# Kernel optimization log

Hardware: AMD Instinct MI355X
Metric: run time of the kernel (lower is better)

## Reference

```python
import jax, jax.numpy as jnp
import numpy as np

N_NODES, N_EDGES, NUM_GRAPHS = 50000, 800000, 64
F_DIM, H_DIM, N_LAYERS, N_CLASSES = 64, 64, 3, 16
EPS = 1e-5  # StdAggregation epsilon (PyG)


def setup_inputs() -> dict:
    key = jax.random.key(0)
    ks = jax.random.split(key, 12)
    s = 0.05
    x = jax.random.normal(ks[0], (N_NODES, F_DIM), jnp.float32)
    edge_index = jax.random.randint(ks[1], (2, N_EDGES), 0, N_NODES, dtype=jnp.int32)
    batch = jnp.sort(jax.random.randint(ks[2], (N_NODES,), 0, NUM_GRAPHS, dtype=jnp.int32))
    # per-layer PNAConv params (towers=1): pre Linear(2F->F), post Linear(13F->H), lin Linear(H->H)
    pre_w = jax.random.normal(ks[3], (N_LAYERS, F_DIM, 2 * F_DIM), jnp.float32) * s
    pre_b = jnp.zeros((N_LAYERS, F_DIM), jnp.float32)
    post_w = jax.random.normal(ks[4], (N_LAYERS, H_DIM, 13 * F_DIM), jnp.float32) * s
    post_b = jnp.zeros((N_LAYERS, H_DIM), jnp.float32)
    lin_w = jax.random.normal(ks[5], (N_LAYERS, H_DIM, H_DIM), jnp.float32) * s
    lin_b = jnp.zeros((N_LAYERS, H_DIM), jnp.float32)
    mlp_w1 = jax.random.normal(ks[6], (H_DIM, H_DIM), jnp.float32) * s
    mlp_b1 = jnp.zeros((H_DIM,), jnp.float32)
    mlp_w2 = jax.random.normal(ks[7], (N_CLASSES, H_DIM), jnp.float32) * s
    mlp_b2 = jnp.zeros((N_CLASSES,), jnp.float32)
    return dict(x=x, edge_index=edge_index, batch=batch,
                pre_w=pre_w, pre_b=pre_b, post_w=post_w, post_b=post_b,
                lin_w=lin_w, lin_b=lin_b, mlp_w1=mlp_w1, mlp_b1=mlp_b1,
                mlp_w2=mlp_w2, mlp_b2=mlp_b2)


def pna_forward(x, src, dst, pre_w, pre_b, post_w, post_b, lin_w, lin_b,
                mlp_w1, mlp_b1, mlp_w2, mlp_b2, batch):
    N = x.shape[0]
    deg_raw = jax.ops.segment_sum(jnp.ones_like(src, jnp.float32), dst, N)  # in-degree [N]
    deg = jnp.maximum(deg_raw, 1.0)[:, None]
    # avg log degree (PNA avg_deg['log'] from the degree histogram of this graph)
    avg_log = jnp.mean(jnp.log(deg_raw + 1.0))
    log_deg = jnp.log(deg + 1.0)
    amp = log_deg / avg_log          # amplification scaler [N,1]
    att = avg_log / log_deg          # attenuation scaler [N,1]
    has_in = (deg_raw > 0)[:, None]

    for l in range(pre_w.shape[0]):
        h = jnp.concatenate([x[dst], x[src]], axis=-1)        # [E, 2F] (x_i, x_j)
        m = h @ pre_w[l].T + pre_b[l]                          # pre_nn message [E, F]
        s1 = jax.ops.segment_sum(m, dst, N)
        s2 = jax.ops.segment_sum(m * m, dst, N)
        mean = s1 / deg
        std = jnp.sqrt(jax.nn.relu(s2 / deg - mean * mean) + EPS)
        mn = jnp.where(has_in, jax.ops.segment_min(m, dst, N), 0.0)
        mx = jnp.where(has_in, jax.ops.segment_max(m, dst, N), 0.0)
        aggr = jnp.concatenate([mean, mn, mx, std], axis=-1)   # [N, 4F]
        out = jnp.concatenate([x, aggr, aggr * amp, aggr * att], axis=-1)  # [N, 13F]
        out = out @ post_w[l].T + post_b[l]                    # post_nn [N, H]
        x = jax.nn.relu(out @ lin_w[l].T + lin_b[l])           # conv.lin + outer ReLU

    # global mean pool over graphs
    counts = jnp.maximum(
        jax.ops.segment_sum(jnp.ones((N,), x.dtype), batch, NUM_GRAPHS), 1.0)
    g = jax.ops.segment_sum(x, batch, NUM_GRAPHS) / counts[:, None]  # [G, H]
    g = jax.nn.relu(g @ mlp_w1.T + mlp_b1)
    return g @ mlp_w2.T + mlp_b2                               # [G, C]


def reference(x, edge_index, batch, pre_w, pre_b, post_w, post_b,
              lin_w, lin_b, mlp_w1, mlp_b1, mlp_w2, mlp_b2):
    src, dst = edge_index[0], edge_index[1]
    return pna_forward(x, src, dst, pre_w, pre_b, post_w, post_b,
                       lin_w, lin_b, mlp_w1, mlp_b1, mlp_w2, mlp_b2, batch)
```

## Files before the change

kernel.cpp:

```cpp
#include <hip/hip_runtime.h>
#include <math.h>

#define N_NODES   50000
#define N_EDGES   800000
#define NUM_GRAPHS 64
#define FDIM      64
#define HDIM      64
#define NLAYERS   3
#define NCLASSES  16
#define EPS       1e-5f

#define SCAN_CHUNK 1024
#define NCHUNKS ((N_NODES + SCAN_CHUNK - 1) / SCAN_CHUNK)

typedef unsigned short u16;
typedef unsigned int   u32;
typedef __attribute__((ext_vector_type(8))) short short8;
typedef __attribute__((ext_vector_type(4))) float floatx4;

#define WKS_LAYER 159744

__device__ inline void split1(float f, u16& h, u16& m, u16& l) {
    u32 b  = __float_as_uint(f);
    u32 hb = b & 0xFFFF0000u;
    float r = f - __uint_as_float(hb);
    u32 mb = __float_as_uint(r) & 0xFFFF0000u;
    float r2 = r - __uint_as_float(mb);
    u32 lb = __float_as_uint(r2) & 0xFFFF0000u;
    h = (u16)(hb >> 16); m = (u16)(mb >> 16); l = (u16)(lb >> 16);
}

__device__ inline void gl_lds16(const void* g, void* l) {
    __builtin_amdgcn_global_load_lds(
        (const __attribute__((address_space(1))) u32*)g,
        (__attribute__((address_space(3))) u32*)l, 16, 0, 0);
}

__global__ __launch_bounds__(256) void k_comb(const float* __restrict__ post_w,
                                              const float* __restrict__ lin_w,
                                              const float* __restrict__ post_b,
                                              const float* __restrict__ lin_b,
                                              u16* __restrict__ WkS,
                                              float* __restrict__ bcv,
                                              int* __restrict__ cnt,
                                              float* __restrict__ logsum) {
    int b = blockIdx.x, t = threadIdx.x;
    int zi = b * 256 + t;
    if (zi < N_NODES) cnt[zi] = 0;
    if (zi == 0) *logsum = 0.f;

    if (b < 624) {
        int c  = t & 63;
        int kl = t >> 6;
        int l  = b / 208;
        int o  = (b % 208) * 4 + kl;
        const float* lw = lin_w + (size_t)l * 4096 + c * 64;
        const float* pw = post_w + (size_t)l * 53248 + o;
        float acc = 0.f;
        #pragma unroll 8
        for (int j = 0; j < 64; ++j)
            acc += lw[j] * pw[(size_t)j * 832];
        u16 h, m, lo;
        split1(acc, h, m, lo);

        int kn;
        if (o < 64) kn = o;
        else {
            int s  = (o - 64) >> 8;
            int mm = (o - 64) & 255;
            int j  = mm >> 5, r = mm & 31;
            kn = 64 + j * 96 + s * 32 + r;
        }
        int ch  = kn >> 5;
        int kin = kn & 31;
        int n16 = c & 15, nt = c >> 4;
        int swk = (((kin >> 3) + (n16 >> 1)) & 3) * 8 + (kin & 7);
        size_t base = (size_t)l * WKS_LAYER + (size_t)ch * 6144
                    + nt * 512 + n16 * 32 + swk;
        WkS[base]        = h;
        WkS[base + 2048] = m;
        WkS[base + 4096] = lo;
    } else if (t < 192) {
        int l = t >> 6, c = t & 63;
        float acc = lin_b[l * 64 + c];
        for (int j = 0; j < 64; ++j)
            acc += lin_w[(size_t)l * 4096 + c * 64 + j] * post_b[l * 64 + j];
        bcv[l * 64 + c] = acc;
    }
}

__global__ void k_count(const int* __restrict__ dst, int* __restrict__ cnt,
                        int* __restrict__ rank) {
    int e = blockIdx.x * 256 + threadIdx.x;
    if (e < N_EDGES) rank[e] = atomicAdd(&cnt[dst[e]], 1);
}

__global__ void k_chunk_sums(const int* __restrict__ cnt, int* __restrict__ bsum,
                             float* __restrict__ logsum) {
    __shared__ int   ired[256];
    __shared__ float lred[256];
    int b = blockIdx.x, t = threadIdx.x;
    int base = b * SCAN_CHUNK;
    int s = 0; float ls = 0.f;
    for (int i = t; i < SCAN_CHUNK; i += 256) {
        int idx = base + i;
        if (idx < N_NODES) {
            int v = cnt[idx];
            s += v;
            ls += logf((float)v + 1.0f);
        }
    }
    ired[t] = s; lred[t] = ls;
    __syncthreads();
    for (int off = 128; off > 0; off >>= 1) {
        if (t < off) { ired[t] += ired[t + off]; lred[t] += lred[t + off]; }
        __syncthreads();
    }
    if (t == 0) { bsum[b] = ired[0]; atomicAdd(logsum, lred[0]); }
}

__global__ void k_scan_top(const int* __restrict__ bsum, int* __restrict__ boff,
                           int* __restrict__ row_start) {
    if (threadIdx.x == 0) {
        int acc = 0;
        for (int i = 0; i < NCHUNKS; ++i) { boff[i] = acc; acc += bsum[i]; }
        row_start[N_NODES] = acc;
    }
}

__global__ void k_scan_chunks(const int* __restrict__ cnt, const int* __restrict__ boff,
                              int* __restrict__ row_start) {
    __shared__ int tsum[256];
    int b = blockIdx.x, t = threadIdx.x;
    int base = b * SCAN_CHUNK + t * 4;
    int v[4]; int s = 0;
    #pragma unroll
    for (int i = 0; i < 4; ++i) {
        int idx = base + i;
        v[i] = (idx < N_NODES) ? cnt[idx] : 0;
        s += v[i];
    }
    tsum[t] = s;
    __syncthreads();
    for (int off = 1; off < 256; off <<= 1) {
        int val = (t >= off) ? tsum[t - off] : 0;
        __syncthreads();
        tsum[t] += val;
        __syncthreads();
    }
    int excl = boff[b] + tsum[t] - s;
    #pragma unroll
    for (int i = 0; i < 4; ++i) {
        int idx = base + i;
        if (idx < N_NODES) row_start[idx] = excl;
        excl += v[i];
    }
}

__global__ void k_scatter(const int* __restrict__ src, const int* __restrict__ dst,
                          const int* __restrict__ rank,
                          const int* __restrict__ row_start,
                          int* __restrict__ csr_src) {
    int e = blockIdx.x * 256 + threadIdx.x;
    if (e < N_EDGES) {
        int d = dst[e];
        csr_src[row_start[d] + rank[e]] = src[e];
    }
}

__global__ void k_scal(const int* __restrict__ cnt, const float* __restrict__ logsum,
                       float* __restrict__ inv_deg, float* __restrict__ ampv,
                       float* __restrict__ attv, float* __restrict__ g_sum,
                       int* __restrict__ g_cnt) {
    int n = blockIdx.x * 256 + threadIdx.x;
    if (blockIdx.x == 0) {
        for (int i = threadIdx.x; i < 4096; i += 256) g_sum[i] = 0.f;
        if (threadIdx.x < 64) g_cnt[threadIdx.x] = 0;
    }
    if (n < N_NODES) {
        float avg = logsum[0] / (float)N_NODES;
        float degf = fmaxf((float)cnt[n], 1.0f);
        inv_deg[n] = 1.0f / degf;
        float ld = logf(degf + 1.0f);
        ampv[n] = ld / avg;
        attv[n] = avg / ld;
    }
}

__global__ __launch_bounds__(256) void k_pre(const float* __restrict__ x,
                                             const float* __restrict__ pre_w,
                                             const float* __restrict__ pre_b,
                                             float* __restrict__ p,
                                             float* __restrict__ q) {
    __shared__ float At[64][68];
    __shared__ float Wt[128][68];
    int t = threadIdx.x;
    int c4 = (t & 15) * 4;
    int r4 = (t >> 4) * 4;
    int rowBase = blockIdx.x * 64;
    int srow = t >> 2, skq = t & 3;

    #pragma unroll
    for (int pass = 0; pass < 4; ++pass) {
        int kk = (pass * 4 + skq) * 4;
        int row = rowBase + srow;
        float4 v = make_float4(0.f, 0.f, 0.f, 0.f);
        if (row < N_NODES) v = *(const float4*)&x[(size_t)row * 64 + kk];
        At[kk + 0][srow] = v.x;
        At[kk + 1][srow] = v.y;
        At[kk + 2][srow] = v.z;
        At[kk + 3][srow] = v.w;
    }
    for (int idx4 = t; idx4 < 2048; idx4 += 256) {
        int c = idx4 & 63, kq = idx4 >> 6;
        float4 v = *(const float4*)&pre_w[(size_t)c * 128 + kq * 4];
        Wt[kq * 4 + 0][c] = v.x;
        Wt[kq * 4 + 1][c] = v.y;
        Wt[kq * 4 + 2][c] = v.z;
        Wt[kq * 4 + 3][c] = v.w;
    }
    __syncthreads();

    float accp[4][4] = {{0}}, accq[4][4] = {{0}};
    #pragma unroll 4
    for (int kk = 0; kk < 64; ++kk) {
        float4 a  = *(const float4*)&At[kk][r4];
        float4 wp = *(const float4*)&Wt[kk][c4];
        float4 wq = *(const float4*)&Wt[64 + kk][c4];
        float av[4]  = {a.x, a.y, a.z, a.w};
        float wpv[4] = {wp.x, wp.y, wp.z, wp.w};
        float wqv[4] = {wq.x, wq.y, wq.z, wq.w};
        #pragma unroll
        for (int i = 0; i < 4; ++i)
            #pragma unroll
            for (int j = 0; j < 4; ++j) {
                accp[i][j] += av[i] * wpv[j];
                accq[i][j] += av[i] * wqv[j];
            }
    }
    float pb[4];
    #pragma unroll
    for (int j = 0; j < 4; ++j) pb[j] = pre_b[c4 + j];
    #pragma unroll
    for (int i = 0; i < 4; ++i) {
        int row = rowBase + r4 + i;
        if (row < N_NODES) {
            float4 vp = make_float4(accp[i][0] + pb[0], accp[i][1] + pb[1],
                                    accp[i][2] + pb[2], accp[i][3] + pb[3]);
            float4 vq = make_float4(accq[i][0], accq[i][1], accq[i][2], accq[i][3]);
            *(float4*)&p[row * 64 + c4] = vp;
            *(float4*)&q[row * 64 + c4] = vq;
        }
    }
}

__global__ __launch_bounds__(256) void k_aggr(const float* __restrict__ p,
                                              const float* __restrict__ q,
                                              const int* __restrict__ row_start,
                                              const int* __restrict__ csr_src,
                                              const float* __restrict__ inv_deg,
                                              float* __restrict__ aggr) {
    int wid  = (blockIdx.x * 256 + threadIdx.x) >> 6;
    int lane = threadIdx.x & 63;
    if (wid >= N_NODES) return;
    int n = wid;
    int beg = row_start[n], end = row_start[n + 1];
    float sum = 0.f, sq = 0.f;
    float mn = INFINITY, mx = -INFINITY;
    int e = beg;
    for (; e + 7 < end; e += 8) {
        float qv[8];
        #pragma unroll
        for (int u = 0; u < 8; ++u) {
            int s = csr_src[e + u];
            qv[u] = q[(size_t)s * 64 + lane];
        }
        #pragma unroll
        for (int u = 0; u < 8; ++u) {
            float m = qv[u];
            sum += m; sq += m * m;
            mn = fminf(mn, m); mx = fmaxf(mx, m);
        }
    }
    for (; e + 3 < end; e += 4) {
        float qv[4];
        #pragma unroll
        for (int u = 0; u < 4; ++u) {
            int s = csr_src[e + u];
            qv[u] = q[(size_t)s * 64 + lane];
        }
        #pragma unroll
        for (int u = 0; u < 4; ++u) {
            float m = qv[u];
            sum += m; sq += m * m;
            mn = fminf(mn, m); mx = fmaxf(mx, m);
        }
    }
    for (; e < end; ++e) {
        int s = csr_src[e];
        float m = q[(size_t)s * 64 + lane];
        sum += m; sq += m * m;
        mn = fminf(mn, m); mx = fmaxf(mx, m);
    }
    float* a = aggr + (size_t)n * 256;
    if (end <= beg) {
        a[lane]       = 0.f;
        a[64 + lane]  = 0.f;
        a[128 + lane] = 0.f;
        a[192 + lane] = sqrtf(EPS);
    } else {
        float pv = p[n * 64 + lane];
        float id = inv_deg[n];
        float meanq = sum * id;
        float var = fmaxf(sq * id - meanq * meanq, 0.f);
        a[lane]       = pv + meanq;
        a[64 + lane]  = pv + mn;
        a[128 + lane] = pv + mx;
        a[192 + lane] = sqrtf(var + EPS);
    }
}

__global__ __launch_bounds__(256, 4) void k_post(const float* __restrict__ x,
                                                 const float* __restrict__ aggr,
                                                 const float* __restrict__ ampv,
                                                 const float* __restrict__ attv,
                                                 const u16* __restrict__ WkS,
                                                 const float* __restrict__ bc,
                                                 float* __restrict__ xout) {
    __shared__ u16 ldsB[2 * 6144];
    int t = threadIdx.x;
    int w = t >> 6;
    int lane = t & 63;
    int m = lane & 15;
    int qh = lane >> 4;
    int rowBase = blockIdx.x * 64;

    int myrow = rowBase + 16 * w + m;
    bool vr = myrow < N_NODES;
    float ampR = vr ? ampv[myrow] : 0.f;
    float attR = vr ? attv[myrow] : 0.f;
    const float* xrow = x + (size_t)(vr ? myrow : 0) * 64;
    const float* arow = aggr + (size_t)(vr ? myrow : 0) * 256;

    int bo = m * 32 + ((qh + (m >> 1)) & 3) * 8;

    floatx4 acc[4] = {};
    float fc[8], fn[8];
    #pragma unroll
    for (int i = 0; i < 8; ++i) { fc[i] = 0.f; fn[i] = 0.f; }

    auto stageIssue = [&](int ch, int buf) {
        const char* g = (const char*)WkS + (size_t)ch * 12288 + w * 3072 + lane * 16;
        char* l = (char*)ldsB + buf * 12288 + w * 3072;
        #pragma unroll
        for (int i = 0; i < 3; ++i)
            gl_lds16(g + i * 1024, l + i * 1024);
    };
    auto loadRaw = [&](const float* sp, float* f) {
        if (!vr) {
            #pragma unroll
            for (int i = 0; i < 8; ++i) f[i] = 0.f;
            return;
        }
        float4 u0 = *(const float4*)sp;
        float4 u1 = *(const float4*)(sp + 4);
        f[0] = u0.x; f[1] = u0.y; f[2] = u0.z; f[3] = u0.w;
        f[4] = u1.x; f[5] = u1.y; f[6] = u1.z; f[7] = u1.w;
    };

    stageIssue(0, 0);
    loadRaw(xrow + qh * 8, fc);
    asm volatile("s_waitcnt vmcnt(0)" ::: "memory");
    __syncthreads();

    for (int ch = 0; ch < 26; ++ch) {
        if (ch + 1 < 26) stageIssue(ch + 1, (ch + 1) & 1);

        if (ch == 0)      loadRaw(xrow + 32 + qh * 8, fn);
        else if (ch == 1) loadRaw(arow + qh * 8, fn);
        else {
            int j = (ch - 2) / 3, s = (ch - 2) % 3;
            if (s == 2 && j < 7) loadRaw(arow + (j + 1) * 32 + qh * 8, fn);
        }

        float sc = 1.f;
        if (ch >= 2) {
            int s = (ch - 2) % 3;
            sc = (s == 0) ? 1.f : ((s == 1) ? ampR : attR);
        }

        union { u32 u[4]; short8 s8; } AH, AM, AL;
        #pragma unroll
        for (int i = 0; i < 4; ++i) {
            float f0 = fc[2 * i] * sc, f1 = fc[2 * i + 1] * sc;
            u32 b0 = __float_as_uint(f0), b1 = __float_as_uint(f1);
            u32 h0 = b0 & 0xFFFF0000u,  h1 = b1 & 0xFFFF0000u;
            float r0 = f0 - __uint_as_float(h0);
            float r1 = f1 - __uint_as_float(h1);
            u32 m0 = __float_as_uint(r0) & 0xFFFF0000u;
            u32 m1 = __float_as_uint(r1) & 0xFFFF0000u;
            float s0 = r0 - __uint_as_float(m0);
            float s1 = r1 - __uint_as_float(m1);
            u32 l0 = __float_as_uint(s0) & 0xFFFF0000u;
            u32 l1 = __float_as_uint(s1) & 0xFFFF0000u;
            AH.u[i] = (h0 >> 16) | h1;
            AM.u[i] = (m0 >> 16) | m1;
            AL.u[i] = (l0 >> 16) | l1;
        }

        const u16* Bb = ldsB + (ch & 1) * 6144;
        #pragma unroll
        for (int nt = 0; nt < 4; ++nt) {
            short8 bH = *(const short8*)(Bb + nt * 512 + bo);
            short8 bM = *(const short8*)(Bb + 2048 + nt * 512 + bo);
            short8 bL = *(const short8*)(Bb + 4096 + nt * 512 + bo);
            acc[nt] = __builtin_amdgcn_mfma_f32_16x16x32_bf16(AH.s8, bH, acc[nt], 0, 0, 0);
            acc[nt] = __builtin_amdgcn_mfma_f32_16x16x32_bf16(AH.s8, bM, acc[nt], 0, 0, 0);
            acc[nt] = __builtin_amdgcn_mfma_f32_16x16x32_bf16(AM.s8, bH, acc[nt], 0, 0, 0);
            acc[nt] = __builtin_amdgcn_mfma_f32_16x16x32_bf16(AH.s8, bL, acc[nt], 0, 0, 0);
            acc[nt] = __builtin_amdgcn_mfma_f32_16x16x32_bf16(AM.s8, bM, acc[nt], 0, 0, 0);
            acc[nt] = __builtin_amdgcn_mfma_f32_16x16x32_bf16(AL.s8, bH, acc[nt], 0, 0, 0);
        }

        asm volatile("s_waitcnt vmcnt(0)" ::: "memory");
        __syncthreads();

        bool adv = (ch < 2) || ((ch - 2) % 3 == 2);
        if (adv) {
            #pragma unroll
            for (int i = 0; i < 8; ++i) fc[i] = fn[i];
        }
    }

    int col = lane & 15;
    #pragma unroll
    for (int nt = 0; nt < 4; ++nt) {
        float bias = bc[nt * 16 + col];
        #pragma unroll
        for (int reg = 0; reg < 4; ++reg) {
            int grow = rowBase + 16 * w + qh * 4 + reg;
            if (grow < N_NODES) {
                xout[(size_t)grow * 64 + nt * 16 + col] =
                    fmaxf(acc[nt][reg] + bias, 0.f);
            }
        }
    }
}

__global__ __launch_bounds__(256) void k_pool(const float* __restrict__ x,
                                              const int* __restrict__ batch,
                                              float* __restrict__ g_sum,
                                              int* __restrict__ g_cnt) {
    int lane = threadIdx.x & 63;
    int wave = blockIdx.x * 4 + (threadIdx.x >> 6);
    const int NPW = 16;
    int beg = wave * NPW;
    if (beg >= N_NODES) return;
    int end = min(beg + NPW, N_NODES);
    float acc = 0.f;
    int cur = batch[beg];
    int c = 0;
    for (int n = beg; n < end; ++n) {
        int b = batch[n];
        if (b != cur) {
            atomicAdd(&g_sum[cur * 64 + lane], acc);
            if (lane == 0) atomicAdd(&g_cnt[cur], c);
            acc = 0.f; c = 0; cur = b;
        }
        acc += x[n * 64 + lane];
        ++c;
    }
    atomicAdd(&g_sum[cur * 64 + lane], acc);
    if (lane == 0) atomicAdd(&g_cnt[cur], c);
}

__global__ __launch_bounds__(256) void k_mlp(const float* __restrict__ g_sum,
                                             const int* __restrict__ g_cnt,
                                             const float* __restrict__ w1,
                                             const float* __restrict__ b1,
                                             const float* __restrict__ w2,
                                             const float* __restrict__ b2,
                                             float* __restrict__ out) {
    __shared__ float g[64][64];
    __shared__ float h[64][64];
    __shared__ float wT[64][65];
    int t = threadIdx.x;
    for (int idx = t; idx < 4096; idx += 256) {
        int gi = idx >> 6, c = idx & 63;
        float cntf = fmaxf((float)g_cnt[gi], 1.f);
        g[gi][c] = g_sum[idx] / cntf;
    }
    for (int idx = t; idx < 4096; idx += 256) {
        int c = idx >> 6, k = idx & 63;
        wT[k][c] = w1[c * 64 + k];
    }
    __syncthreads();
    for (int idx = t; idx < 4096; idx += 256) {
        int gi = idx >> 6, c = idx & 63;
        float acc = b1[c];
        for (int k = 0; k < 64; ++k) acc += g[gi][k] * wT[k][c];
        h[gi][c] = fmaxf(acc, 0.f);
    }
    __syncthreads();
    for (int idx = t; idx < 64 * NCLASSES; idx += 256) {
        int gi = idx >> 4, c = idx & 15;
        float acc = b2[c];
        for (int k = 0; k < 64; ++k) acc += h[gi][k] * w2[c * 64 + k];
        out[gi * NCLASSES + c] = acc;
    }
}

extern "C" void kernel_launch(void* const* d_in, const int* in_sizes, int n_in,
                              void* d_out, int out_size, void* d_ws, size_t ws_size,
                              hipStream_t stream) {
    const float* x      = (const float*)d_in[0];
    const int*   ei     = (const int*)d_in[1];
    const int*   batch  = (const int*)d_in[2];
    const float* pre_w  = (const float*)d_in[3];
    const float* pre_b  = (const float*)d_in[4];
    const float* post_w = (const float*)d_in[5];
    const float* post_b = (const float*)d_in[6];
    const float* lin_w  = (const float*)d_in[7];
    const float* lin_b  = (const float*)d_in[8];
    const float* mlp_w1 = (const float*)d_in[9];
    const float* mlp_b1 = (const float*)d_in[10];
    const float* mlp_w2 = (const float*)d_in[11];
    const float* mlp_b2 = (const float*)d_in[12];

    const int* src = ei;
    const int* dst = ei + N_EDGES;

    char* base = (char*)d_ws;
    size_t off = 0;
    auto alloc = [&](size_t bytes) -> void* {
        void* ptr = base + off;
        off += (bytes + 255) & ~(size_t)255;
        return ptr;
    };
    int*   cnt       = (int*)alloc(N_NODES * 4);
    int*   row_start = (int*)alloc((N_NODES + 1) * 4);
    int*   rank      = (int*)alloc(N_EDGES * 4);
    int*   csr_src   = (int*)alloc(N_EDGES * 4);
    int*   bsum      = (int*)alloc(64 * 4);
    int*   boff      = (int*)alloc(64 * 4);
    float* logsum    = (float*)alloc(16);
    float* inv_deg   = (float*)alloc(N_NODES * 4);
    float* ampv      = (float*)alloc(N_NODES * 4);
    float* attv      = (float*)alloc(N_NODES * 4);
    float* p         = (float*)alloc((size_t)N_NODES * 64 * 4);
    float* q         = (float*)alloc((size_t)N_NODES * 64 * 4);
    float* aggr      = (float*)alloc((size_t)N_NODES * 256 * 4);
    float* xb0       = (float*)alloc((size_t)N_NODES * 64 * 4);
    float* xb1       = (float*)alloc((size_t)N_NODES * 64 * 4);
    float* g_sum     = (float*)alloc(64 * 64 * 4);
    int*   g_cnt     = (int*)alloc(64 * 4);
    u16*   WkS       = (u16*)alloc((size_t)3 * WKS_LAYER * 2);
    float* bcv       = (float*)alloc(3 * 64 * 4);

    k_comb<<<625, 256, 0, stream>>>(post_w, lin_w, post_b, lin_b, WkS, bcv,
                                    cnt, logsum);

    k_count<<<(N_EDGES + 255) / 256, 256, 0, stream>>>(dst, cnt, rank);
    k_chunk_sums<<<NCHUNKS, 256, 0, stream>>>(cnt, bsum, logsum);
    k_scan_top<<<1, 64, 0, stream>>>(bsum, boff, row_start);
    k_scan_chunks<<<NCHUNKS, 256, 0, stream>>>(cnt, boff, row_start);
    k_scatter<<<(N_EDGES + 255) / 256, 256, 0, stream>>>(src, dst, rank,
                                                         row_start, csr_src);
    k_scal<<<(N_NODES + 255) / 256, 256, 0, stream>>>(cnt, logsum, inv_deg,
                                                      ampv, attv, g_sum, g_cnt);

    const int GEMM_BLOCKS = (N_NODES + 63) / 64;
    const float* xin = x;
    float* bufs[3] = {xb0, xb1, xb0};
    for (int l = 0; l < NLAYERS; ++l) {
        k_pre<<<GEMM_BLOCKS, 256, 0, stream>>>(xin, pre_w + (size_t)l * 64 * 128,
                                               pre_b + l * 64, p, q);
        k_aggr<<<(N_NODES + 3) / 4, 256, 0, stream>>>(p, q, row_start, csr_src,
                                                      inv_deg, aggr);
        float* xo = bufs[l];
        k_post<<<GEMM_BLOCKS, 256, 0, stream>>>(xin, aggr, ampv, attv,
                                                WkS + (size_t)l * WKS_LAYER,
                                                bcv + l * 64, xo);
        xin = xo;
    }

    int pool_waves = (N_NODES + 15) / 16;
    k_pool<<<(pool_waves + 3) / 4, 256, 0, stream>>>(xin, batch, g_sum, g_cnt);
    k_mlp<<<1, 256, 0, stream>>>(g_sum, g_cnt, mlp_w1, mlp_b1, mlp_w2, mlp_b2,
                                 (float*)d_out);
}
```

Baseline: 492.4 us.

## Triple-buffer post-GEMM weight staging with partial vmcnt waits in k_post

Moves the k_post weight staging from a double-buffered LDS scheme to a triple-buffered one. Each chunk prefetches the weights two chunks ahead and waits with a partial vmcnt count instead of draining all outstanding loads before the barrier. The activation loads are made unconditional, issued every chunk through a pointer helper that repeats addresses, and masked afterward, so the fixed count of outstanding memory ops stays valid. This adds LDS use, which may cut occupancy, and issues redundant global loads plus wrap-around prefetches of early chunks.

```diff
diff --git a/kernel.cpp b/kernel.cpp
--- a/kernel.cpp
+++ b/kernel.cpp
@@ -327,7 +327,7 @@
                                                  const u16* __restrict__ WkS,
                                                  const float* __restrict__ bc,
                                                  float* __restrict__ xout) {
-    __shared__ u16 ldsB[2 * 6144];
+    __shared__ u16 ldsB[3 * 6144];
     int t = threadIdx.x;
     int w = t >> 6;
     int lane = t & 63;
@@ -337,18 +337,32 @@
 
     int myrow = rowBase + 16 * w + m;
     bool vr = myrow < N_NODES;
-    float ampR = vr ? ampv[myrow] : 0.f;
-    float attR = vr ? attv[myrow] : 0.f;
-    const float* xrow = x + (size_t)(vr ? myrow : 0) * 64;
-    const float* arow = aggr + (size_t)(vr ? myrow : 0) * 256;
+    int crow = vr ? myrow : 0;
+    float ampR = vr ? ampv[crow] : 0.f;
+    float attR = vr ? attv[crow] : 0.f;
+    const float* xrow = x + (size_t)crow * 64;
+    const float* arow = aggr + (size_t)crow * 256;
 
     int bo = m * 32 + ((qh + (m >> 1)) & 3) * 8;
 
     floatx4 acc[4] = {};
     float fc[8], fn[8];
-    #pragma unroll
-    for (int i = 0; i < 8; ++i) { fc[i] = 0.f; fn[i] = 0.f; }
-
+
+    auto aptr = [&](int ch) -> const float* {
+        if (ch <= 0) return xrow;
+        if (ch == 1) return xrow + 32;
+        int j = (ch - 2) / 3;
+        if (j > 7) j = 7;
+        return arow + j * 32;
+    };
+    auto loadRaw = [&](const float* sp, float* f) {
+        float4 u0 = *(const float4*)(sp + qh * 8);
+        float4 u1 = *(const float4*)(sp + qh * 8 + 4);
+        f[0] = vr ? u0.x : 0.f; f[1] = vr ? u0.y : 0.f;
+        f[2] = vr ? u0.z : 0.f; f[3] = vr ? u0.w : 0.f;
+        f[4] = vr ? u1.x : 0.f; f[5] = vr ? u1.y : 0.f;
+        f[6] = vr ? u1.z : 0.f; f[7] = vr ? u1.w : 0.f;
+    };
     auto stageIssue = [&](int ch, int buf) {
         const char* g = (const char*)WkS + (size_t)ch * 12288 + w * 3072 + lane * 16;
         char* l = (char*)ldsB + buf * 12288 + w * 3072;
@@ -356,32 +370,17 @@
         for (int i = 0; i < 3; ++i)
             gl_lds16(g + i * 1024, l + i * 1024);
     };
-    auto loadRaw = [&](const float* sp, float* f) {
-        if (!vr) {
-            #pragma unroll
-            for (int i = 0; i < 8; ++i) f[i] = 0.f;
-            return;
-        }
-        float4 u0 = *(const float4*)sp;
-        float4 u1 = *(const float4*)(sp + 4);
-        f[0] = u0.x; f[1] = u0.y; f[2] = u0.z; f[3] = u0.w;
-        f[4] = u1.x; f[5] = u1.y; f[6] = u1.z; f[7] = u1.w;
-    };
-
+
+    loadRaw(aptr(0), fc);
     stageIssue(0, 0);
-    loadRaw(xrow + qh * 8, fc);
-    asm volatile("s_waitcnt vmcnt(0)" ::: "memory");
-    __syncthreads();
+    stageIssue(1, 1);
+    asm volatile("s_waitcnt vmcnt(3)" ::: "memory");
+    asm volatile("s_barrier" ::: "memory");
 
     for (int ch = 0; ch < 26; ++ch) {
-        if (ch + 1 < 26) stageIssue(ch + 1, (ch + 1) & 1);
-
-        if (ch == 0)      loadRaw(xrow + 32 + qh * 8, fn);
-        else if (ch == 1) loadRaw(arow + qh * 8, fn);
-        else {
-            int j = (ch - 2) / 3, s = (ch - 2) % 3;
-            if (s == 2 && j < 7) loadRaw(arow + (j + 1) * 32 + qh * 8, fn);
-        }
+        loadRaw(aptr(ch + 1), fn);
+        int ch2 = (ch + 2 < 26) ? ch + 2 : ch + 2 - 26;
+        stageIssue(ch2, (ch + 2) % 3);
 
         float sc = 1.f;
         if (ch >= 2) {
@@ -408,7 +407,7 @@
             AL.u[i] = (l0 >> 16) | l1;
         }
 
-        const u16* Bb = ldsB + (ch & 1) * 6144;
+        const u16* Bb = ldsB + (ch % 3) * 6144;
         #pragma unroll
         for (int nt = 0; nt < 4; ++nt) {
             short8 bH = *(const short8*)(Bb + nt * 512 + bo);
@@ -422,14 +421,11 @@
             acc[nt] = __builtin_amdgcn_mfma_f32_16x16x32_bf16(AL.s8, bH, acc[nt], 0, 0, 0);
         }
 
-        asm volatile("s_waitcnt vmcnt(0)" ::: "memory");
-        __syncthreads();
-
-        bool adv = (ch < 2) || ((ch - 2) % 3 == 2);
-        if (adv) {
-            #pragma unroll
-            for (int i = 0; i < 8; ++i) fc[i] = fn[i];
-        }
+        asm volatile("s_waitcnt vmcnt(5)" ::: "memory");
+        asm volatile("s_barrier" ::: "memory");
+
+        #pragma unroll
+        for (int i = 0; i < 8; ++i) fc[i] = fn[i];
     }
 
     int col = lane & 15;
```

Measured after the change: 491.5 us. About the same (-0.2%).
